# Optimization experiments

Measured on AMD Instinct MI355X. Metric: run time of the kernel, lower is better.

Reference implementation:

```python
import jax, jax.numpy as jnp
import numpy as np

AVG_STEP_WEIGHTING = 0.002


def _mean_rbf_kernel(a, b):
    """Mean over all (i,j) of exp(-||a_i - b_j||^2 / 2), features flattened.

    Equivalent to the original per-row loop: (1/N) * sum_i mean_j k(b, a_i).
    Uses the Gram trick to avoid materializing (N, M, D) intermediates.
    """
    A = a.reshape(a.shape[0], -1)  # (N, D)
    B = b.reshape(b.shape[0], -1)  # (M, D)
    sq_a = jnp.sum(A * A, axis=1)  # (N,)
    sq_b = jnp.sum(B * B, axis=1)  # (M,)
    # (N, M) pairwise squared distances; clamp tiny negatives from fp error
    d2 = jnp.maximum(sq_a[:, None] + sq_b[None, :] - 2.0 * (A @ B.T), 0.0)
    return jnp.mean(jnp.exp(-0.5 * d2))


def setup_inputs() -> dict:
    key = jax.random.key(0)
    kx, ky = jax.random.split(key)
    N, M, D1, D2 = 4096, 4096, 24, 8
    x = jax.random.normal(kx, (N, D1, D2), dtype=jnp.float32)
    y = jax.random.normal(ky, (M, D1, D2), dtype=jnp.float32)
    avg_step = jnp.asarray(5.0, dtype=jnp.float32)
    return {"x": x, "y": y, "avg_step": avg_step}


def reference(x, y, avg_step):
    XX = _mean_rbf_kernel(x, x)
    XY = _mean_rbf_kernel(x, y)
    YY = _mean_rbf_kernel(y, y)
    mmd = XX + YY - 2.0 * XY
    loss = mmd + (jnp.maximum(jnp.asarray(1.0, x.dtype), avg_step) - 1.0) * AVG_STEP_WEIGHTING
    return (loss, mmd)
```

## Files before the change

kernel.cpp:

```cpp
#include <hip/hip_runtime.h>
#include <hip/hip_bf16.h>

typedef __attribute__((ext_vector_type(8))) short short8;
typedef __attribute__((ext_vector_type(4))) float float4v;
typedef __attribute__((ext_vector_type(4))) short short4v;

#define N_ROWS 4096
#define K_DIM  192
#define TILE   128
#define NT     32
#define NSYM   528
#define NBLK   2080
#define C1     (-0.72134752044448179f)
#define LOG2E  (1.4426950408889634f)

__device__ __forceinline__ void gl16(const short* g, short* l)
{
    __builtin_amdgcn_global_load_lds((const __attribute__((address_space(1))) void*)g,
                                     (__attribute__((address_space(3))) void*)l,
                                     16, 0, 0);
}

__global__ void prep_kernel(const float* __restrict__ x, const float* __restrict__ y,
                            __hip_bfloat16* __restrict__ xb, __hip_bfloat16* __restrict__ yb,
                            float* __restrict__ sqx, float* __restrict__ sqy)
{
    int w    = (blockIdx.x * blockDim.x + threadIdx.x) >> 6;
    int lane = threadIdx.x & 63;
    if (w >= 2 * N_ROWS) return;
    const float* src = (w < N_ROWS) ? (x + (size_t)w * K_DIM) : (y + (size_t)(w - N_ROWS) * K_DIM);
    short*       dst = (short*)((w < N_ROWS) ? (xb + (size_t)w * K_DIM)
                                             : (yb + (size_t)(w - N_ROWS) * K_DIM));
    float s = 0.f;
    if (lane < 48) {
        float4v v = *(const float4v*)(src + lane * 4);
        short4v h;
        #pragma unroll
        for (int i = 0; i < 4; ++i) {
            __hip_bfloat16 b = __float2bfloat16(v[i]);
            h[i] = *(short*)&b;
            float fb = __bfloat162float(b);
            s += fb * fb;
        }
        *(short4v*)(dst + lane * 4) = h;
    }
    #pragma unroll
    for (int off = 32; off; off >>= 1) s += __shfl_down(s, off, 64);
    if (lane == 0) {
        if (w < N_ROWS) sqx[w] = s; else sqy[w - N_ROWS] = s;
    }
}

__global__ __launch_bounds__(256) void gram_kernel(const __hip_bfloat16* __restrict__ xb,
                            const __hip_bfloat16* __restrict__ yb,
                            const float* __restrict__ sqx, const float* __restrict__ sqy,
                            float* __restrict__ partials)
{
    __shared__ short lds[16384];
    __shared__ float wred[4];

    const short* xbs = (const short*)xb;
    const short* ybs = (const short*)yb;

    int id = blockIdx.x;
    const short *A, *B; const float *sa, *sb;
    int bi, bj;
    float weight = 1.0f;
    if (id < 2 * NSYM) {
        int t;
        if (id < NSYM) { t = id;        A = xbs; B = xbs; sa = sqx; sb = sqx; }
        else           { t = id - NSYM; A = ybs; B = ybs; sa = sqy; sb = sqy; }
        bi = 0;
        while (t >= NT - bi) { t -= NT - bi; ++bi; }
        bj = bi + t;
        if (bi != bj) weight = 2.0f;
    } else {
        int t = id - 2 * NSYM;
        bi = t >> 5; bj = t & 31;
        A = xbs; B = ybs; sa = sqx; sb = sqy;
    }
    const int abase = bi * TILE, bbase = bj * TILE;

    const int tid  = threadIdx.x;
    const int lane = tid & 63, w = tid >> 6;
    const int wm   = w >> 1,  wn = w & 1;
    const int m15  = lane & 15, quad = lane >> 4;

    const int crow = tid >> 2;
    const int xch  = (tid & 3) ^ (crow & 3);
    const short* srcA = A + (size_t)(abase + crow) * K_DIM + xch * 8;
    const short* srcB = B + (size_t)(bbase + crow) * K_DIM + xch * 8;

    const int slotq = ((quad ^ (m15 & 3)) * 8);
    int aoff[4], boff[4];
    #pragma unroll
    for (int tm = 0; tm < 4; ++tm) aoff[tm] = (wm * 64 + tm * 16 + m15) * 32 + slotq;
    #pragma unroll
    for (int tn = 0; tn < 4; ++tn) boff[tn] = (wn * 64 + tn * 16 + m15) * 32 + slotq;

    float4v acc[4][4];
    #pragma unroll
    for (int i = 0; i < 4; ++i)
        #pragma unroll
        for (int j = 0; j < 4; ++j) acc[i][j] = (float4v){0.f, 0.f, 0.f, 0.f};

#define STAGE(p, k0)                                                         \
    {                                                                        \
        short* da = lds + (p) * 8192 + (tid & 0xC0) * 8;        \
        gl16(srcA + (k0),               da);               \
        gl16(srcA + (k0) + 64 * K_DIM,  da + 2048);        \
        short* db = da + 4096;                                               \
        gl16(srcB + (k0),               db);                                 \
        gl16(srcB + (k0) + 64 * K_DIM,  db + 2048);                          \
    }

#define COMPUTE(p)                                                           \
    {                                                                        \
        const short* a0 = lds + (p) * 8192;                                  \
        const short* b0 = a0 + 4096;                                         \
        short8 af[4], bfr[4];                                                \
        _Pragma("unroll")                                                    \
        for (int tm = 0; tm < 4; ++tm) af[tm]  = *(const short8*)(a0 + aoff[tm]); \
        _Pragma("unroll")                                                    \
        for (int tn = 0; tn < 4; ++tn) bfr[tn] = *(const short8*)(b0 + boff[tn]); \
        _Pragma("unroll")                                                    \
        for (int tm = 0; tm < 4; ++tm)                                       \
            _Pragma("unroll")                                                \
            for (int tn = 0; tn < 4; ++tn)                                   \
                acc[tm][tn] = __builtin_amdgcn_mfma_f32_16x16x32_bf16(af[tm], bfr[tn], acc[tm][tn], 0, 0, 0); \
    }

    STAGE(0, 0)
    __syncthreads();
    #pragma unroll
    for (int s = 1; s <= 5; ++s) {
        STAGE(s & 1, s * 32)
        COMPUTE((s - 1) & 1)
        __syncthreads();
    }
    COMPUTE(1)

#undef STAGE
#undef COMPUTE

    float u[16], v[4];
    #pragma unroll
    for (int tm = 0; tm < 4; ++tm)
        #pragma unroll
        for (int r = 0; r < 4; ++r)
            u[tm * 4 + r] = C1 * sa[abase + wm * 64 + tm * 16 + quad * 4 + r];
    #pragma unroll
    for (int tn = 0; tn < 4; ++tn)
        v[tn] = C1 * sb[bbase + wn * 64 + tn * 16 + m15];

    float lsum = 0.f;
    #pragma unroll
    for (int tm = 0; tm < 4; ++tm)
        #pragma unroll
        for (int tn = 0; tn < 4; ++tn)
            #pragma unroll
            for (int r = 0; r < 4; ++r) {
                float g  = acc[tm][tn][r];
                float sv = fminf(u[tm * 4 + r] + v[tn] + LOG2E * g, 0.f);
                lsum += exp2f(sv);
            }

    #pragma unroll
    for (int off = 32; off; off >>= 1) lsum += __shfl_down(lsum, off, 64);
    if (lane == 0) wred[w] = lsum;
    __syncthreads();
    if (tid == 0) partials[id] = weight * (wred[0] + wred[1] + wred[2] + wred[3]);
}

__global__ void final_kernel(const float* __restrict__ partials, const float* __restrict__ avg_step,
                             float* __restrict__ out)
{
    __shared__ float red[3][4];
    int tid = threadIdx.x, lane = tid & 63, w = tid >> 6;
    float s0 = 0.f, s1 = 0.f, s2 = 0.f;
    for (int i = tid; i < NSYM; i += 256) s0 += partials[i];
    for (int i = tid; i < NSYM; i += 256) s1 += partials[NSYM + i];
    for (int i = tid; i < 1024; i += 256) s2 += partials[2 * NSYM + i];
    #pragma unroll
    for (int off = 32; off; off >>= 1) {
        s0 += __shfl_down(s0, off, 64);
        s1 += __shfl_down(s1, off, 64);
        s2 += __shfl_down(s2, off, 64);
    }
    if (lane == 0) { red[0][w] = s0; red[1][w] = s1; red[2][w] = s2; }
    __syncthreads();
    if (tid == 0) {
        float sxx = red[0][0] + red[0][1] + red[0][2] + red[0][3];
        float syy = red[1][0] + red[1][1] + red[1][2] + red[1][3];
        float sxy = red[2][0] + red[2][1] + red[2][2] + red[2][3];
        const float inv = 1.0f / 16777216.0f;
        float XX = sxx * inv, YY = syy * inv, XY = sxy * inv;
        float mmd  = XX + YY - 2.0f * XY;
        float stepv = fmaxf(1.0f, avg_step[0]);
        float loss = mmd + (stepv - 1.0f) * 0.002f;
        out[0] = loss;
        out[1] = mmd;
    }
}

extern "C" void kernel_launch(void* const* d_in, const int* in_sizes, int n_in,
                              void* d_out, int out_size, void* d_ws, size_t ws_size,
                              hipStream_t stream)
{
    const float* x        = (const float*)d_in[0];
    const float* y        = (const float*)d_in[1];
    const float* avg_step = (const float*)d_in[2];

    char* ws = (char*)d_ws;
    __hip_bfloat16* xb       = (__hip_bfloat16*)(ws);
    __hip_bfloat16* yb       = (__hip_bfloat16*)(ws + 1572864);
    float*          sqx      = (float*)(ws + 3145728);
    float*          sqy      = (float*)(ws + 3162112);
    float*          partials = (float*)(ws + 3178496);

    prep_kernel<<<2048, 256, 0, stream>>>(x, y, xb, yb, sqx, sqy);
    gram_kernel<<<NBLK, 256, 0, stream>>>(xb, yb, sqx, sqy, partials);
    final_kernel<<<1, 256, 0, stream>>>(partials, avg_step, (float*)d_out);
}
```

Measured before the change: 90.80 us.

## Use 256x256 tiles with 512 threads and fuse final reduction via atomic ticket

Doubles the Gram tile to 256x256 per block with 8 waves, each computing a 128x64 sub-tile. This cuts the block count from 2080 to 528 and raises operand reuse per LDS load. It also removes the separate final kernel: each block atomically adds its partial into per-matrix accumulators, and the last block, found through a ticket counter, writes the loss. The risks are higher register pressure (32 accumulator fragments), fewer blocks for load balancing across CUs, and non-deterministic float atomic summation order.

Result: slower. 105.1 us (+15.8%).

```diff
diff --git a/kernel.cpp b/kernel.cpp
--- a/kernel.cpp
+++ b/kernel.cpp
@@ -7,10 +7,10 @@
 
 #define N_ROWS 4096
 #define K_DIM  192
-#define TILE   128
-#define NT     32
-#define NSYM   528
-#define NBLK   2080
+#define TILE   256
+#define NT     16
+#define NSYM   136
+#define NBLK   528
 #define C1     (-0.72134752044448179f)
 #define LOG2E  (1.4426950408889634f)
 
@@ -23,8 +23,13 @@
 
 __global__ void prep_kernel(const float* __restrict__ x, const float* __restrict__ y,
                             __hip_bfloat16* __restrict__ xb, __hip_bfloat16* __restrict__ yb,
-                            float* __restrict__ sqx, float* __restrict__ sqy)
-{
+                            float* __restrict__ sqx, float* __restrict__ sqy,
+                            float* __restrict__ accum, unsigned* __restrict__ ticket)
+{
+    if (blockIdx.x == 0) {
+        if (threadIdx.x < 3) accum[threadIdx.x] = 0.f;
+        if (threadIdx.x == 3) *ticket = 0u;
+    }
     int w    = (blockIdx.x * blockDim.x + threadIdx.x) >> 6;
     int lane = threadIdx.x & 63;
     if (w >= 2 * N_ROWS) return;
@@ -51,39 +56,40 @@
     }
 }
 
-__global__ __launch_bounds__(256) void gram_kernel(const __hip_bfloat16* __restrict__ xb,
+__global__ __launch_bounds__(512) void gram_kernel(const __hip_bfloat16* __restrict__ xb,
                             const __hip_bfloat16* __restrict__ yb,
                             const float* __restrict__ sqx, const float* __restrict__ sqy,
-                            float* __restrict__ partials)
-{
-    __shared__ short lds[16384];
-    __shared__ float wred[4];
+                            float* __restrict__ accum, unsigned* __restrict__ ticket,
+                            const float* __restrict__ avg_step, float* __restrict__ out)
+{
+    __shared__ short lds[32768];
+    __shared__ float wred[8];
 
     const short* xbs = (const short*)xb;
     const short* ybs = (const short*)yb;
 
     int id = blockIdx.x;
     const short *A, *B; const float *sa, *sb;
-    int bi, bj;
+    int bi, bj, sel;
     float weight = 1.0f;
     if (id < 2 * NSYM) {
         int t;
-        if (id < NSYM) { t = id;        A = xbs; B = xbs; sa = sqx; sb = sqx; }
-        else           { t = id - NSYM; A = ybs; B = ybs; sa = sqy; sb = sqy; }
+        if (id < NSYM) { t = id;        A = xbs; B = xbs; sa = sqx; sb = sqx; sel = 0; }
+        else           { t = id - NSYM; A = ybs; B = ybs; sa = sqy; sb = sqy; sel = 1; }
         bi = 0;
         while (t >= NT - bi) { t -= NT - bi; ++bi; }
         bj = bi + t;
         if (bi != bj) weight = 2.0f;
     } else {
         int t = id - 2 * NSYM;
-        bi = t >> 5; bj = t & 31;
-        A = xbs; B = ybs; sa = sqx; sb = sqy;
+        bi = t >> 4; bj = t & 15;
+        A = xbs; B = ybs; sa = sqx; sb = sqy; sel = 2;
     }
     const int abase = bi * TILE, bbase = bj * TILE;
 
     const int tid  = threadIdx.x;
     const int lane = tid & 63, w = tid >> 6;
-    const int wm   = w >> 1,  wn = w & 1;
+    const int wm   = w >> 2,  wn = w & 3;
     const int m15  = lane & 15, quad = lane >> 4;
 
     const int crow = tid >> 2;
@@ -91,42 +97,41 @@
     const short* srcA = A + (size_t)(abase + crow) * K_DIM + xch * 8;
     const short* srcB = B + (size_t)(bbase + crow) * K_DIM + xch * 8;
 
-    const int slotq = ((quad ^ (m15 & 3)) * 8);
-    int aoff[4], boff[4];
-    #pragma unroll
-    for (int tm = 0; tm < 4; ++tm) aoff[tm] = (wm * 64 + tm * 16 + m15) * 32 + slotq;
+    const int slotq = (quad ^ (m15 & 3)) * 8;
+    int aoff[8], boff[4];
+    #pragma unroll
+    for (int tm = 0; tm < 8; ++tm) aoff[tm] = (wm * 128 + tm * 16 + m15) * 32 + slotq;
     #pragma unroll
     for (int tn = 0; tn < 4; ++tn) boff[tn] = (wn * 64 + tn * 16 + m15) * 32 + slotq;
 
-    float4v acc[4][4];
-    #pragma unroll
-    for (int i = 0; i < 4; ++i)
+    float4v acc[8][4];
+    #pragma unroll
+    for (int i = 0; i < 8; ++i)
         #pragma unroll
         for (int j = 0; j < 4; ++j) acc[i][j] = (float4v){0.f, 0.f, 0.f, 0.f};
 
-#define STAGE(p, k0)                                                         \
-    {                                                                        \
-        short* da = lds + (p) * 8192 + (tid & 0xC0) * 8;        \
-        gl16(srcA + (k0),               da);               \
-        gl16(srcA + (k0) + 64 * K_DIM,  da + 2048);        \
-        short* db = da + 4096;                                               \
-        gl16(srcB + (k0),               db);                                 \
-        gl16(srcB + (k0) + 64 * K_DIM,  db + 2048);                          \
-    }
-
-#define COMPUTE(p)                                                           \
-    {                                                                        \
-        const short* a0 = lds + (p) * 8192;                                  \
-        const short* b0 = a0 + 4096;                                         \
-        short8 af[4], bfr[4];                                                \
-        _Pragma("unroll")                                                    \
-        for (int tm = 0; tm < 4; ++tm) af[tm]  = *(const short8*)(a0 + aoff[tm]); \
-        _Pragma("unroll")                                                    \
+#define STAGE(p, k0)                                                          \
+    {                                                                         \
+        short* d = lds + (p) * 16384 + (tid & 0x1C0) * 8;        \
+        gl16(srcA + (k0),                d);             \
+        gl16(srcA + (k0) + 128 * K_DIM,  d + 4096);      \
+        gl16(srcB + (k0),                d + 8192);      \
+        gl16(srcB + (k0) + 128 * K_DIM,  d + 12288);     \
+    }
+
+#define COMPUTE(p)                                                            \
+    {                                                                         \
+        const short* a0 = lds + (p) * 16384;                                  \
+        const short* b0 = a0 + 8192;                                          \
+        short8 af[8], bfr[4];                                                 \
+        _Pragma("unroll")                                                     \
+        for (int tm = 0; tm < 8; ++tm) af[tm]  = *(const short8*)(a0 + aoff[tm]); \
+        _Pragma("unroll")                                                     \
         for (int tn = 0; tn < 4; ++tn) bfr[tn] = *(const short8*)(b0 + boff[tn]); \
-        _Pragma("unroll")                                                    \
-        for (int tm = 0; tm < 4; ++tm)                                       \
-            _Pragma("unroll")                                                \
-            for (int tn = 0; tn < 4; ++tn)                                   \
+        _Pragma("unroll")                                                     \
+        for (int tm = 0; tm < 8; ++tm)                                        \
+            _Pragma("unroll")                                                 \
+            for (int tn = 0; tn < 4; ++tn)                                    \
                 acc[tm][tn] = __builtin_amdgcn_mfma_f32_16x16x32_bf16(af[tm], bfr[tn], acc[tm][tn], 0, 0, 0); \
     }
 
@@ -143,63 +148,50 @@
 #undef STAGE
 #undef COMPUTE
 
-    float u[16], v[4];
-    #pragma unroll
-    for (int tm = 0; tm < 4; ++tm)
-        #pragma unroll
-        for (int r = 0; r < 4; ++r)
-            u[tm * 4 + r] = C1 * sa[abase + wm * 64 + tm * 16 + quad * 4 + r];
+    float v[4];
     #pragma unroll
     for (int tn = 0; tn < 4; ++tn)
         v[tn] = C1 * sb[bbase + wn * 64 + tn * 16 + m15];
 
     float lsum = 0.f;
     #pragma unroll
-    for (int tm = 0; tm < 4; ++tm)
+    for (int tm = 0; tm < 8; ++tm) {
+        float u[4];
+        #pragma unroll
+        for (int r = 0; r < 4; ++r)
+            u[r] = C1 * sa[abase + wm * 128 + tm * 16 + quad * 4 + r];
         #pragma unroll
         for (int tn = 0; tn < 4; ++tn)
             #pragma unroll
             for (int r = 0; r < 4; ++r) {
                 float g  = acc[tm][tn][r];
-                float sv = fminf(u[tm * 4 + r] + v[tn] + LOG2E * g, 0.f);
+                float sv = fminf(u[r] + v[tn] + LOG2E * g, 0.f);
                 lsum += exp2f(sv);
             }
+    }
 
     #pragma unroll
     for (int off = 32; off; off >>= 1) lsum += __shfl_down(lsum, off, 64);
     if (lane == 0) wred[w] = lsum;
     __syncthreads();
-    if (tid == 0) partials[id] = weight * (wred[0] + wred[1] + wred[2] + wred[3]);
-}
-
-__global__ void final_kernel(const float* __restrict__ partials, const float* __restrict__ avg_step,
-                             float* __restrict__ out)
-{
-    __shared__ float red[3][4];
-    int tid = threadIdx.x, lane = tid & 63, w = tid >> 6;
-    float s0 = 0.f, s1 = 0.f, s2 = 0.f;
-    for (int i = tid; i < NSYM; i += 256) s0 += partials[i];
-    for (int i = tid; i < NSYM; i += 256) s1 += partials[NSYM + i];
-    for (int i = tid; i < 1024; i += 256) s2 += partials[2 * NSYM + i];
-    #pragma unroll
-    for (int off = 32; off; off >>= 1) {
-        s0 += __shfl_down(s0, off, 64);
-        s1 += __shfl_down(s1, off, 64);
-        s2 += __shfl_down(s2, off, 64);
-    }
-    if (lane == 0) { red[0][w] = s0; red[1][w] = s1; red[2][w] = s2; }
-    __syncthreads();
     if (tid == 0) {
-        float sxx = red[0][0] + red[0][1] + red[0][2] + red[0][3];
-        float syy = red[1][0] + red[1][1] + red[1][2] + red[1][3];
-        float sxy = red[2][0] + red[2][1] + red[2][2] + red[2][3];
-        const float inv = 1.0f / 16777216.0f;
-        float XX = sxx * inv, YY = syy * inv, XY = sxy * inv;
-        float mmd  = XX + YY - 2.0f * XY;
-        float stepv = fmaxf(1.0f, avg_step[0]);
-        float loss = mmd + (stepv - 1.0f) * 0.002f;
-        out[0] = loss;
-        out[1] = mmd;
+        float bsum = weight * (wred[0] + wred[1] + wred[2] + wred[3] +
+                               wred[4] + wred[5] + wred[6] + wred[7]);
+        atomicAdd(&accum[sel], bsum);
+        __threadfence();
+        unsigned old = atomicAdd(ticket, 1u);
+        if (old == NBLK - 1) {
+            __threadfence();
+            float sxx = atomicAdd(&accum[0], 0.f);
+            float syy = atomicAdd(&accum[1], 0.f);
+            float sxy = atomicAdd(&accum[2], 0.f);
+            const float inv = 1.0f / 16777216.0f;
+            float XX = sxx * inv, YY = syy * inv, XY = sxy * inv;
+            float mmd  = XX + YY - 2.0f * XY;
+            float stepv = fmaxf(1.0f, avg_step[0]);
+            out[0] = mmd + (stepv - 1.0f) * 0.002f;
+            out[1] = mmd;
+        }
     }
 }
 
@@ -216,9 +208,10 @@
     __hip_bfloat16* yb       = (__hip_bfloat16*)(ws + 1572864);
     float*          sqx      = (float*)(ws + 3145728);
     float*          sqy      = (float*)(ws + 3162112);
-    float*          partials = (float*)(ws + 3178496);
-
-    prep_kernel<<<2048, 256, 0, stream>>>(x, y, xb, yb, sqx, sqy);
-    gram_kernel<<<NBLK, 256, 0, stream>>>(xb, yb, sqx, sqy, partials);
-    final_kernel<<<1, 256, 0, stream>>>(partials, avg_step, (float*)d_out);
-}
+    float*          accum    = (float*)(ws + 3178496);
+    unsigned*       ticket   = (unsigned*)(ws + 3178508);
+
+    prep_kernel<<<2048, 256, 0, stream>>>(x, y, xb, yb, sqx, sqy, accum, ticket);
+    gram_kernel<<<NBLK, 512, 0, stream>>>(xb, yb, sqx, sqy, accum, ticket,
+                                          avg_step, (float*)d_out);
+}
```

## Load A fragments to registers, stage full B tile in LDS, remap block ids

Applied to the files above, without the earlier changes.

Each wave now loads its 32-row slice of the A tile straight from global memory into registers for the full K=192. The whole 128x192 B tile is staged into LDS in one pass with an XOR swizzle, replacing the double-buffered K loop and its five barriers with a single barrier. Block ids are permuted across eight groups, likely to spread work over XCDs or improve L2 locality, and MFMA priority is raised during the compute loop. The cost is more LDS per block (48KB), which may lower occupancy, and uncoalesced-per-row global loads for A.

Result: no change. 91.18 us (+0.4%).

```diff
diff --git a/kernel.cpp b/kernel.cpp
--- a/kernel.cpp
+++ b/kernel.cpp
@@ -56,13 +56,14 @@
                             const float* __restrict__ sqx, const float* __restrict__ sqy,
                             float* __restrict__ partials)
 {
-    __shared__ short lds[16384];
+    __shared__ short lB[24576];
     __shared__ float wred[4];
 
     const short* xbs = (const short*)xb;
     const short* ybs = (const short*)yb;
 
-    int id = blockIdx.x;
+    int id = (blockIdx.x & 7) * 260 + (blockIdx.x >> 3);
+
     const short *A, *B; const float *sa, *sb;
     int bi, bj;
     float weight = 1.0f;
@@ -83,87 +84,78 @@
 
     const int tid  = threadIdx.x;
     const int lane = tid & 63, w = tid >> 6;
-    const int wm   = w >> 1,  wn = w & 1;
     const int m15  = lane & 15, quad = lane >> 4;
 
-    const int crow = tid >> 2;
-    const int xch  = (tid & 3) ^ (crow & 3);
-    const short* srcA = A + (size_t)(abase + crow) * K_DIM + xch * 8;
-    const short* srcB = B + (size_t)(bbase + crow) * K_DIM + xch * 8;
-
-    const int slotq = ((quad ^ (m15 & 3)) * 8);
-    int aoff[4], boff[4];
-    #pragma unroll
-    for (int tm = 0; tm < 4; ++tm) aoff[tm] = (wm * 64 + tm * 16 + m15) * 32 + slotq;
-    #pragma unroll
-    for (int tn = 0; tn < 4; ++tn) boff[tn] = (wn * 64 + tn * 16 + m15) * 32 + slotq;
-
-    float4v acc[4][4];
-    #pragma unroll
-    for (int i = 0; i < 4; ++i)
-        #pragma unroll
-        for (int j = 0; j < 4; ++j) acc[i][j] = (float4v){0.f, 0.f, 0.f, 0.f};
-
-#define STAGE(p, k0)                                                         \
-    {                                                                        \
-        short* da = lds + (p) * 8192 + (tid & 0xC0) * 8;        \
-        gl16(srcA + (k0),               da);               \
-        gl16(srcA + (k0) + 64 * K_DIM,  da + 2048);        \
-        short* db = da + 4096;                                               \
-        gl16(srcB + (k0),               db);                                 \
-        gl16(srcB + (k0) + 64 * K_DIM,  db + 2048);                          \
-    }
-
-#define COMPUTE(p)                                                           \
-    {                                                                        \
-        const short* a0 = lds + (p) * 8192;                                  \
-        const short* b0 = a0 + 4096;                                         \
-        short8 af[4], bfr[4];                                                \
-        _Pragma("unroll")                                                    \
-        for (int tm = 0; tm < 4; ++tm) af[tm]  = *(const short8*)(a0 + aoff[tm]); \
-        _Pragma("unroll")                                                    \
-        for (int tn = 0; tn < 4; ++tn) bfr[tn] = *(const short8*)(b0 + boff[tn]); \
-        _Pragma("unroll")                                                    \
-        for (int tm = 0; tm < 4; ++tm)                                       \
-            _Pragma("unroll")                                                \
-            for (int tn = 0; tn < 4; ++tn)                                   \
-                acc[tm][tn] = __builtin_amdgcn_mfma_f32_16x16x32_bf16(af[tm], bfr[tn], acc[tm][tn], 0, 0, 0); \
-    }
-
-    STAGE(0, 0)
+    short8 af[2][6];
+    #pragma unroll
+    for (int tm = 0; tm < 2; ++tm) {
+        const short* ar = A + (size_t)(abase + w * 32 + tm * 16 + m15) * K_DIM + quad * 8;
+        #pragma unroll
+        for (int ks = 0; ks < 6; ++ks)
+            af[tm][ks] = *(const short8*)(ar + ks * 32);
+    }
+
+    #pragma unroll
+    for (int r = 0; r < 12; ++r) {
+        int c    = r * 256 + tid;
+        int row  = (c & 511) >> 2;
+        int slot = c & 3;
+        int xsl  = slot ^ (row & 3) ^ ((row >> 2) & 3);
+        const short* src = B + (size_t)(bbase + row) * K_DIM + (c >> 9) * 32 + xsl * 8;
+        short* dst = lB + (r >> 1) * 4096 + (((r & 1) << 8) + (w << 6)) * 8;
+        gl16(src, dst);
+    }
+
+    float4v acc[2][8];
+    #pragma unroll
+    for (int i = 0; i < 2; ++i)
+        #pragma unroll
+        for (int j = 0; j < 8; ++j) acc[i][j] = (float4v){0.f, 0.f, 0.f, 0.f};
+
     __syncthreads();
-    #pragma unroll
-    for (int s = 1; s <= 5; ++s) {
-        STAGE(s & 1, s * 32)
-        COMPUTE((s - 1) & 1)
-        __syncthreads();
-    }
-    COMPUTE(1)
-
-#undef STAGE
-#undef COMPUTE
-
-    float u[16], v[4];
-    #pragma unroll
-    for (int tm = 0; tm < 4; ++tm)
+
+    const int rsw = (quad ^ (m15 & 3) ^ ((m15 >> 2) & 3)) << 3;
+    __builtin_amdgcn_s_setprio(1);
+    #pragma unroll
+    for (int ks = 0; ks < 6; ++ks) {
+        const short* b0 = lB + ks * 4096 + rsw;
+        #pragma unroll
+        for (int h = 0; h < 2; ++h) {
+            short8 bf[4];
+            #pragma unroll
+            for (int j = 0; j < 4; ++j)
+                bf[j] = *(const short8*)(b0 + (h * 64 + j * 16 + m15) * 32);
+            #pragma unroll
+            for (int tm = 0; tm < 2; ++tm)
+                #pragma unroll
+                for (int j = 0; j < 4; ++j)
+                    acc[tm][h * 4 + j] = __builtin_amdgcn_mfma_f32_16x16x32_bf16(
+                        af[tm][ks], bf[j], acc[tm][h * 4 + j], 0, 0, 0);
+        }
+    }
+    __builtin_amdgcn_s_setprio(0);
+
+    float v[8];
+    #pragma unroll
+    for (int tn = 0; tn < 8; ++tn)
+        v[tn] = C1 * sb[bbase + tn * 16 + m15];
+
+    float lsum = 0.f;
+    #pragma unroll
+    for (int tm = 0; tm < 2; ++tm) {
+        float u[4];
         #pragma unroll
         for (int r = 0; r < 4; ++r)
-            u[tm * 4 + r] = C1 * sa[abase + wm * 64 + tm * 16 + quad * 4 + r];
-    #pragma unroll
-    for (int tn = 0; tn < 4; ++tn)
-        v[tn] = C1 * sb[bbase + wn * 64 + tn * 16 + m15];
-
-    float lsum = 0.f;
-    #pragma unroll
-    for (int tm = 0; tm < 4; ++tm)
-        #pragma unroll
-        for (int tn = 0; tn < 4; ++tn)
+            u[r] = C1 * sa[abase + w * 32 + tm * 16 + quad * 4 + r];
+        #pragma unroll
+        for (int tn = 0; tn < 8; ++tn)
             #pragma unroll
             for (int r = 0; r < 4; ++r) {
                 float g  = acc[tm][tn][r];
-                float sv = fminf(u[tm * 4 + r] + v[tn] + LOG2E * g, 0.f);
+                float sv = fminf(u[r] + v[tn] + LOG2E * g, 0.f);
                 lsum += exp2f(sv);
             }
+    }
 
     #pragma unroll
     for (int off = 32; off; off >>= 1) lsum += __shfl_down(lsum, off, 64);
```
